# Kernel tuning notes

Hardware: AMD Instinct MI355X
Metric: run time of the kernel (lower is better)

## Reference

```python
import jax, jax.numpy as jnp
import numpy as np

B, T, DKQ, DV, EKQ, EV, H, OUT = 8, 2048, 64, 64, 128, 128, 4, 32
FF = 4 * EV
NEG = -1e30  # additive mask value (safe stand-in for -inf)


def _ln(x, g, b, eps=1e-5):
    m = x.mean(-1, keepdims=True)
    var = ((x - m) ** 2).mean(-1, keepdims=True)
    return (x - m) * jax.lax.rsqrt(var + eps) * g + b


def _attn(q, k, v, mask):
    # q,k,v: [n, T, E] -> heads [n, H, T, dh]; NOTE: no 1/sqrt(d) scaling (faithful to source)
    n, t, _ = q.shape
    q = q.reshape(n, t, H, -1).transpose(0, 2, 1, 3)
    k = k.reshape(n, t, H, -1).transpose(0, 2, 1, 3)
    v = v.reshape(n, t, H, -1).transpose(0, 2, 1, 3)
    w = jnp.einsum('bhqd,bhkd->bhqk', q, k) + mask  # [n,H,T,T]
    a = jax.nn.softmax(w, axis=-1)
    o = jnp.einsum('bhqk,bhkd->bhqd', a, v)
    return o.transpose(0, 2, 1, 3).reshape(n, t, -1)


def setup_inputs() -> dict:
    key = jax.random.key(0)
    ks = jax.random.split(key, 32)
    w = lambda k, s: jax.random.normal(k, s, jnp.float32) * 0.02
    DIN_A = DKQ + DV
    return {
        'kq': jax.random.normal(ks[0], (B, T, DKQ), jnp.float32),
        'v': jax.random.normal(ks[1], (B, T, DV), jnp.float32),
        # Layer A (input_dim = DKQ+DV, embed = EV)
        'A_Wk': w(ks[2], (DIN_A, EV)), 'A_bk': jnp.zeros((EV,), jnp.float32),
        'A_Wq': w(ks[3], (DIN_A, EV)), 'A_bq': jnp.zeros((EV,), jnp.float32),
        'A_Wv': w(ks[4], (DIN_A, EV)), 'A_bv': jnp.zeros((EV,), jnp.float32),
        'A_f1W': w(ks[5], (EV, FF)), 'A_f1b': jnp.zeros((FF,), jnp.float32),
        'A_f2W': w(ks[6], (FF, EV)), 'A_f2b': jnp.zeros((EV,), jnp.float32),
        'A_n1g': jnp.ones((EV,), jnp.float32), 'A_n1b': jnp.zeros((EV,), jnp.float32),
        'A_n2g': jnp.ones((EV,), jnp.float32), 'A_n2b': jnp.zeros((EV,), jnp.float32),
        # Layer B (kq -> EKQ, vA -> EV)
        'B_Wk': w(ks[7], (DKQ, EKQ)), 'B_bk': jnp.zeros((EKQ,), jnp.float32),
        'B_Wq': w(ks[8], (DKQ, EKQ)), 'B_bq': jnp.zeros((EKQ,), jnp.float32),
        'B_Wv': w(ks[9], (EV, EV)), 'B_bv': jnp.zeros((EV,), jnp.float32),
        'B_f1W': w(ks[10], (EV, FF)), 'B_f1b': jnp.zeros((FF,), jnp.float32),
        'B_f2W': w(ks[11], (FF, EV)), 'B_f2b': jnp.zeros((EV,), jnp.float32),
        # Output head
        'out_W': w(ks[12], (EV, OUT)), 'out_b': jnp.zeros((OUT,), jnp.float32),
    }


def reference(kq, v, A_Wk, A_bk, A_Wq, A_bq, A_Wv, A_bv, A_f1W, A_f1b, A_f2W, A_f2b,
              A_n1g, A_n1b, A_n2g, A_n2b, B_Wk, B_bk, B_Wq, B_bq, B_Wv, B_bv,
              B_f1W, B_f1b, B_f2W, B_f2b, out_W, out_b):
    n, t, _ = kq.shape
    i = jnp.arange(t)[:, None]
    j = jnp.arange(t)[None, :]
    mask_a = jnp.where(j <= i, 0.0, NEG).astype(jnp.float32)               # causal (diag=1)
    mask_b = jnp.where((j < i) | ((i == 0) & (j == 0)), 0.0, NEG).astype(jnp.float32)  # strict causal + (0,0) exception

    # ---- Layer A ----
    X = jnp.concatenate([kq, v], axis=-1)
    K = X @ A_Wk + A_bk
    Q = X @ A_Wq + A_bq
    V = X @ A_Wv + A_bv
    attn_out = _attn(Q, K, V, mask_a)
    h1 = _ln(V + attn_out, A_n1g, A_n1b)
    ff = jax.nn.gelu(h1 @ A_f1W + A_f1b, approximate=False) @ A_f2W + A_f2b
    vA = _ln(h1 + ff, A_n2g, A_n2b)

    # ---- Layer B (no residuals / norms: values is overwritten in source) ----
    K2 = kq @ B_Wk + B_bk
    Q2 = kq @ B_Wq + B_bq
    V2 = vA @ B_Wv + B_bv
    attn_out2 = _attn(Q2, K2, V2, mask_b)
    ff2 = jax.nn.gelu(attn_out2 @ B_f1W + B_f1b, approximate=False) @ B_f2W + B_f2b

    return ff2 @ out_W + out_b
```

## Files before the change

kernel.cpp:

```cpp
#include <hip/hip_runtime.h>
#include <hip/hip_bf16.h>

#define TSEQ 2048
#define NBATCH 8
#define NROWS (NBATCH*TSEQ)
#define EMB 128
#define NH 4
#define DH 32
#define OUTD 32
#define APLANE (NROWS*EMB)
#define LOG2E 1.44269504088896340736f
#define NPAR 4

typedef short s8v __attribute__((ext_vector_type(8)));
typedef short s4v __attribute__((ext_vector_type(4)));
typedef float f4v __attribute__((ext_vector_type(4)));
typedef float f16v __attribute__((ext_vector_type(16)));
typedef unsigned int u4v __attribute__((ext_vector_type(4)));

__device__ __forceinline__ unsigned short f2bf(float f){
  unsigned int u = __float_as_uint(f);
  unsigned int r = u + 0x7fffu + ((u >> 16) & 1u);
  return (unsigned short)(r >> 16);
}
__device__ __forceinline__ float bf2f(unsigned short u){
  return __uint_as_float(((unsigned int)u) << 16);
}
__device__ __forceinline__ float exp2fast(float x){
#if __has_builtin(__builtin_amdgcn_exp2f)
  return __builtin_amdgcn_exp2f(x);
#else
  return __expf(x * 0.6931471805599453f);
#endif
}

struct WPack {
  const float* src[10];
  int off[10];
  int ntk[10];
  int rowoff[10];
  int nsh[10];
  int kn[10];
};
__global__ __launch_bounds__(256) void prep(WPack p, short* __restrict__ warena,
                                            const float* __restrict__ kq, const float* __restrict__ v,
                                            unsigned short* __restrict__ X){
  int blk = blockIdx.x;
  if (blk < (NROWS*EMB/256)){
    int idx = blk*256 + threadIdx.x;
    int row = idx >> 7, c = idx & 127;
    float val = (c < 64) ? kq[row*64 + c] : v[row*64 + (c-64)];
    unsigned short hi = f2bf(val);
    X[idx]          = hi;
    X[idx + APLANE] = f2bf(val - bf2f(hi));
    return;
  }
  blk -= (NROWS*EMB/256);
  int m = 0;
  #pragma unroll
  for (int i=0;i<10;i++){
    int nb = p.kn[i] >> 8;
    if (blk < nb){ m = i; break; }
    blk -= nb;
  }
  int idx = blk*256 + threadIdx.x;
  float x = p.src[m][idx];
  int nsh = p.nsh[m];
  int n = idx & ((1<<nsh)-1);
  int k = idx >> nsh;
  int K = p.kn[m] >> nsh;
  unsigned short hi = f2bf(x);
  unsigned short lo = f2bf(x - bf2f(hi));
  short* dh = warena + p.off[m] + (size_t)(p.rowoff[m] + n)*K + k;
  dh[0]        = (short)hi;
  dh[p.ntk[m]] = (short)lo;
}

struct GOuts {
  const float* bias[3];
  float* of[3];
  unsigned short* ob[3];
  float scl[3];
};
template<int CT>
__global__ __launch_bounds__(256) void gemm2(
    const unsigned short* __restrict__ A, int aplane, int lda, int K, int niter,
    const short* __restrict__ wt, int NTK,
    GOuts og, int NT, int nseg, int act,
    unsigned short* __restrict__ vtb, int vcol0){
  __shared__ short As[2][2][64*40];
  const int tid  = threadIdx.x;
  const int w    = tid >> 6;
  const int lane = tid & 63;
  const int col  = lane & 15;
  const int quad = lane >> 4;
  const int row0 = blockIdx.x * 64;
  const int cb   = blockIdx.y*(64*CT) + w*(16*CT) + col;
  const bool two = (aplane != 0);

  f4v acc[4][CT];
  #pragma unroll
  for (int i=0;i<4;i++)
    #pragma unroll
    for (int j=0;j<CT;j++) acc[i][j] = (f4v){0.f,0.f,0.f,0.f};

  const int ar = tid >> 2, ac = (tid & 3)*8;
  const unsigned short* abase = A + (size_t)(row0 + ar)*lda;

  s8v pah, pal;
  pah = *(const s8v*)(abase + ac);
  if (two) pal = *(const s8v*)(abase + aplane + ac);

  const short* wbase[CT];
  #pragma unroll
  for (int ct=0;ct<CT;ct++) wbase[ct] = wt + (size_t)(cb + ct*16)*K + quad*8;

  for (int i=0;i<niter;i++){
    const int buf = i & 1;
    *(s8v*)&As[buf][0][ar*40 + ac] = pah;
    if (two) *(s8v*)&As[buf][1][ar*40 + ac] = pal;
    __syncthreads();
    if (i+1 < niter){
      const int kcol = (i+1)*32 + ac;
      pah = *(const s8v*)(abase + kcol);
      if (two) pal = *(const s8v*)(abase + aplane + kcol);
    }
    s8v bh[CT], bl[CT];
    #pragma unroll
    for (int ct=0;ct<CT;ct++){
      bh[ct] = *(const s8v*)(wbase[ct] + i*32);
      bl[ct] = *(const s8v*)(wbase[ct] + i*32 + NTK);
    }
    #pragma unroll
    for (int rt=0;rt<4;rt++){
      s8v ah = *(const s8v*)&As[buf][0][(rt*16 + col)*40 + quad*8];
      #pragma unroll
      for (int ct=0;ct<CT;ct++)
        acc[rt][ct] = __builtin_amdgcn_mfma_f32_16x16x32_bf16(ah, bh[ct], acc[rt][ct], 0, 0, 0);
      if (two){
        s8v al = *(const s8v*)&As[buf][1][(rt*16 + col)*40 + quad*8];
        #pragma unroll
        for (int ct=0;ct<CT;ct++)
          acc[rt][ct] = __builtin_amdgcn_mfma_f32_16x16x32_bf16(al, bh[ct], acc[rt][ct], 0, 0, 0);
      }
      #pragma unroll
      for (int ct=0;ct<CT;ct++)
        acc[rt][ct] = __builtin_amdgcn_mfma_f32_16x16x32_bf16(ah, bl[ct], acc[rt][ct], 0, 0, 0);
    }
  }

  const int NB = 64*CT;
  const int cb0 = (int)blockIdx.y * NB;
  const bool dotr = (vtb != nullptr) && (cb0 >= vcol0) && (cb0 < vcol0 + 128);
  short* Lt = &As[0][0][0];
  if (dotr) __syncthreads();

  #pragma unroll
  for (int ct=0;ct<CT;ct++){
    const int cg = cb + ct*16;
    int seg, lcol, ldc;
    if (nseg > 1){ seg = cg >> 7; lcol = cg & 127; ldc = 128; }
    else         { seg = 0; lcol = cg; ldc = NT; }
    const float bv = og.bias[seg][lcol];
    const float sc = og.scl[seg];
    float* of = og.of[seg];
    unsigned short* ob = og.ob[seg];
    #pragma unroll
    for (int rt=0;rt<4;rt++){
      s4v pk;
      #pragma unroll
      for (int r=0;r<4;r++){
        const int row = row0 + rt*16 + quad*4 + r;
        float val = acc[rt][ct][r] + bv;
        if (act == 1) val = 0.5f*val*(1.f + erff(val*0.70710678118654752440f));
        val *= sc;
        if (ob)      ob[(size_t)row*ldc + lcol] = f2bf(val);
        else if (of) of[(size_t)row*ldc + lcol] = val;
        if (dotr) pk[r] = (short)f2bf(val);
      }
      if (dotr)
        *(s4v*)&Lt[(w*(16*CT) + ct*16 + col)*72 + rt*16 + quad*4] = pk;
    }
  }
  if (dotr){
    __syncthreads();
    const int b = row0 >> 11, t0 = row0 & 2047;
    #pragma unroll
    for (int it=0; it<2*CT; it++){
      const int cl = it*32 + (tid>>3);
      const int t8 = (tid&7)*8;
      s8v o = *(const s8v*)&Lt[cl*72 + t8];
      const int cr = cb0 + cl - vcol0;
      *(s8v*)(vtb + ((size_t)((b*4 + (cr>>5))*32 + (cr&31)))*2048 + t0 + t8) = o;
    }
  }
}

#define KSTR 40
#define VSTR 72
__device__ __forceinline__ int kswz(int row, int c){ return (row*KSTR + c) ^ (((row>>3)&3)<<3); }
__device__ __forceinline__ int vswz(int row, int c){ return (row*VSTR + c) ^ (((row>>3)&3)<<3); }

__global__ __launch_bounds__(256, 4) void flash5(const unsigned short* __restrict__ Qb,
                                                 const unsigned short* __restrict__ Kb,
                                                 const unsigned short* __restrict__ Vtb,
                                                 float* __restrict__ O, float* __restrict__ L,
                                                 int mode){
  __shared__ short Kt[64*KSTR];
  __shared__ short Vt[32*VSTR];
  const int tid  = threadIdx.x;
  const int w    = tid >> 6;
  const int lane = tid & 63;
  const int q31  = lane & 31;
  const int hi   = lane >> 5;
  const int bh = blockIdx.y;
  const int b = bh >> 2, h = bh & 3;
  const int par = blockIdx.z;
  float* Op = O + (size_t)par*NROWS*EMB;
  float* Lp = L + (size_t)par*NROWS*NH;
  const int kr = tid >> 2, kc8 = (tid & 3)*8;
  const int vd = tid >> 3, vk8 = (tid & 7)*8;

  for (int pass = 0; pass < 2; pass++){
    const int qt = pass ? (int)blockIdx.x : (15 - (int)blockIdx.x);
    const int qbase = qt*128;
    const int qrow  = qbase + w*32 + q31;
    const int jtmax = 2*qt + 1;

    s8v qB0 = *(const s8v*)(Qb + (size_t)(b*TSEQ + qrow)*EMB + h*DH + hi*8);
    s8v qB1 = *(const s8v*)(Qb + (size_t)(b*TSEQ + qrow)*EMB + h*DH + 16 + hi*8);
    f16v o;
    #pragma unroll
    for (int r=0;r<16;r++) o[r] = 0.f;
    float lr = 0.f;

    if (par <= jtmax){
      s8v ka = *(const s8v*)(Kb + (size_t)(b*TSEQ + par*64 + kr)*EMB + h*DH + kc8);
      s8v va = *(const s8v*)(Vtb + ((size_t)bh*32 + vd)*TSEQ + par*64 + vk8);
      for (int jt = par; jt <= jtmax; jt += NPAR){
        __syncthreads();
        *(s8v*)&Kt[kswz(kr, kc8)] = ka;
        *(s8v*)&Vt[vswz(vd, vk8)] = va;
        __syncthreads();
        if (jt + NPAR <= jtmax){
          ka = *(const s8v*)(Kb + (size_t)(b*TSEQ + (jt+NPAR)*64 + kr)*EMB + h*DH + kc8);
          va = *(const s8v*)(Vtb + ((size_t)bh*32 + vd)*TSEQ + (jt+NPAR)*64 + vk8);
        }
        const bool domask = (jt >= 2*qt);
        #pragma unroll
        for (int kt=0;kt<2;kt++){
          f16v s;
          #pragma unroll
          for (int r=0;r<16;r++) s[r] = 0.f;
          {
            s8v kf0 = *(const s8v*)&Kt[kswz(kt*32 + q31, hi*8)];
            s = __builtin_amdgcn_mfma_f32_32x32x16_bf16(kf0, qB0, s, 0, 0, 0);
            s8v kf1 = *(const s8v*)&Kt[kswz(kt*32 + q31, 16 + hi*8)];
            s = __builtin_amdgcn_mfma_f32_32x32x16_bf16(kf1, qB1, s, 0, 0, 0);
          }
          if (domask){
            #pragma unroll
            for (int r=0;r<16;r++){
              const int jg = jt*64 + kt*32 + (r&3) + 8*(r>>2) + 4*hi;
              const bool ok = (mode==0) ? (jg <= qrow) : ((jg < qrow) || (qrow==0 && jg==0));
              s[r] = ok ? s[r] : -1e30f;
            }
          }
          #pragma unroll
          for (int r=0;r<16;r++){ float pv = exp2fast(s[r]); s[r] = pv; lr += pv; }
          unsigned P2[4][2];
          #pragma unroll
          for (int m=0;m<4;m++){
            asm("v_cvt_pk_bf16_f32 %0, %1, %2" : "=v"(P2[m][0]) : "v"(s[4*m+0]), "v"(s[4*m+1]));
            asm("v_cvt_pk_bf16_f32 %0, %1, %2" : "=v"(P2[m][1]) : "v"(s[4*m+2]), "v"(s[4*m+3]));
          }
          #pragma unroll
          for (int kcl=0;kcl<2;kcl++){
            const unsigned own0 = hi ? P2[2*kcl+1][0] : P2[2*kcl][0];
            const unsigned own1 = hi ? P2[2*kcl+1][1] : P2[2*kcl][1];
            const unsigned inv0 = hi ? P2[2*kcl][0]   : P2[2*kcl+1][0];
            const unsigned inv1 = hi ? P2[2*kcl][1]   : P2[2*kcl+1][1];
            const unsigned sx0 = (unsigned)__shfl_xor((int)inv0, 32);
            const unsigned sx1 = (unsigned)__shfl_xor((int)inv1, 32);
            u4v au;
            au[0] = hi ? sx0 : own0;  au[1] = hi ? sx1 : own1;
            au[2] = hi ? own0 : sx0;  au[3] = hi ? own1 : sx1;
            s8v af = __builtin_bit_cast(s8v, au);
            s8v vf = *(const s8v*)&Vt[vswz(q31, kt*32 + kcl*16 + hi*8)];
            o = __builtin_amdgcn_mfma_f32_32x32x16_bf16(af, vf, o, 0, 0, 0);
          }
        }
      }
    }
    const float lt = lr + __shfl_xor(lr, 32);
    #pragma unroll
    for (int r=0;r<16;r++){
      const int ql = (r&3) + 8*(r>>2) + 4*hi;
      Op[(size_t)(b*TSEQ + qbase + w*32 + ql)*EMB + h*DH + q31] = o[r];
    }
    if (hi == 0) Lp[(size_t)(b*TSEQ + qrow)*NH + h] = lt;
  }
}

__global__ __launch_bounds__(256) void combine_ln(const float* __restrict__ O, const float* __restrict__ L,
                                                  const float* __restrict__ Vf,
                                                  const float* __restrict__ g, const float* __restrict__ bt,
                                                  unsigned short* __restrict__ outp){
  const int row = blockIdx.x*4 + (threadIdx.x >> 6);
  const int tid = threadIdx.x & 63;
  const size_t base = (size_t)row*EMB;
  const int h0 = tid >> 5, h1i = 2 + (tid >> 5);
  float la = 0.f, lb = 0.f, s0 = 0.f, s1 = 0.f;
  #pragma unroll
  for (int p=0;p<NPAR;p++){
    la += L[(size_t)p*NROWS*NH + (size_t)row*NH + h0];
    lb += L[(size_t)p*NROWS*NH + (size_t)row*NH + h1i];
    s0 += O[(size_t)p*NROWS*EMB + base + tid];
    s1 += O[(size_t)p*NROWS*EMB + base + tid + 64];
  }
  float x0 = Vf[base+tid]    + s0/la;
  float x1 = Vf[base+tid+64] + s1/lb;
  float s  = x0 + x1;
  float s2 = x0*x0 + x1*x1;
  #pragma unroll
  for (int off=1; off<64; off<<=1){
    s  += __shfl_xor(s,  off);
    s2 += __shfl_xor(s2, off);
  }
  float mean = s * (1.f/128.f);
  float var  = s2 * (1.f/128.f) - mean*mean;
  float rstd = rsqrtf(var + 1e-5f);
  float y0 = (x0-mean)*rstd*g[tid]    + bt[tid];
  float y1 = (x1-mean)*rstd*g[tid+64] + bt[tid+64];
  unsigned short h0b = f2bf(y0), h1b = f2bf(y1);
  outp[base+tid]             = h0b;
  outp[base+tid+64]          = h1b;
  outp[base+tid+APLANE]      = f2bf(y0 - bf2f(h0b));
  outp[base+tid+64+APLANE]   = f2bf(y1 - bf2f(h1b));
}

__global__ __launch_bounds__(256) void ln2(const unsigned short* __restrict__ Xp, const float* __restrict__ R,
                                           const float* __restrict__ g, const float* __restrict__ bt,
                                           unsigned short* __restrict__ outp){
  const int row = blockIdx.x*4 + (threadIdx.x >> 6);
  const int tid = threadIdx.x & 63;
  const size_t base = (size_t)row*EMB;
  float x0 = bf2f(Xp[base+tid])    + bf2f(Xp[base+tid+APLANE])    + R[base+tid];
  float x1 = bf2f(Xp[base+tid+64]) + bf2f(Xp[base+tid+64+APLANE]) + R[base+tid+64];
  float s  = x0 + x1;
  float s2 = x0*x0 + x1*x1;
  #pragma unroll
  for (int off=1; off<64; off<<=1){
    s  += __shfl_xor(s,  off);
    s2 += __shfl_xor(s2, off);
  }
  float mean = s * (1.f/128.f);
  float var  = s2 * (1.f/128.f) - mean*mean;
  float rstd = rsqrtf(var + 1e-5f);
  float y0 = (x0-mean)*rstd*g[tid]    + bt[tid];
  float y1 = (x1-mean)*rstd*g[tid+64] + bt[tid+64];
  unsigned short h0b = f2bf(y0), h1b = f2bf(y1);
  outp[base+tid]             = h0b;
  outp[base+tid+64]          = h1b;
  outp[base+tid+APLANE]      = f2bf(y0 - bf2f(h0b));
  outp[base+tid+64+APLANE]   = f2bf(y1 - bf2f(h1b));
}

__global__ __launch_bounds__(256) void combine_b(const float* __restrict__ O, const float* __restrict__ L,
                                                 unsigned short* __restrict__ outp){
  const int idx = blockIdx.x*256 + threadIdx.x;
  const int row = idx >> 7, c = idx & 127, h = c >> 5;
  float l = 0.f, ov = 0.f;
  #pragma unroll
  for (int p=0;p<NPAR;p++){
    l  += L[(size_t)p*NROWS*NH + (size_t)row*NH + h];
    ov += O[(size_t)p*NROWS*EMB + idx];
  }
  const float v = ov / l;
  unsigned short hb = f2bf(v);
  outp[idx]          = hb;
  outp[idx + APLANE] = f2bf(v - bf2f(hb));
}

__global__ __launch_bounds__(256) void out_proj(const float* __restrict__ A,
                                                const float* __restrict__ W, const float* __restrict__ bb,
                                                float* __restrict__ out){
  __shared__ float As[8*128];
  __shared__ float Ws2[128*32];
  const int tid = threadIdx.x;
  const int row0 = blockIdx.x * 8;
  for (int idx = tid; idx < 8*128; idx += 256) As[idx] = A[(size_t)row0*128 + idx];
  for (int idx = tid; idx < 128*32; idx += 256) Ws2[idx] = W[idx];
  __syncthreads();
  const int r = tid >> 5, c = tid & 31;
  float acc = bb[c];
  #pragma unroll 8
  for (int k=0;k<128;k++) acc = fmaf(As[r*128 + k], Ws2[k*32 + c], acc);
  out[(size_t)(row0 + r)*OUTD + c] = acc;
}

extern "C" void kernel_launch(void* const* d_in, const int* in_sizes, int n_in,
                              void* d_out, int out_size, void* d_ws, size_t ws_size,
                              hipStream_t stream) {
  const float* kq    = (const float*)d_in[0];
  const float* v     = (const float*)d_in[1];
  const float* A_Wk  = (const float*)d_in[2];  const float* A_bk  = (const float*)d_in[3];
  const float* A_Wq  = (const float*)d_in[4];  const float* A_bq  = (const float*)d_in[5];
  const float* A_Wv  = (const float*)d_in[6];  const float* A_bv  = (const float*)d_in[7];
  const float* A_f1W = (const float*)d_in[8];  const float* A_f1b = (const float*)d_in[9];
  const float* A_f2W = (const float*)d_in[10]; const float* A_f2b = (const float*)d_in[11];
  const float* A_n1g = (const float*)d_in[12]; const float* A_n1b = (const float*)d_in[13];
  const float* A_n2g = (const float*)d_in[14]; const float* A_n2b = (const float*)d_in[15];
  const float* B_Wk  = (const float*)d_in[16]; const float* B_bk  = (const float*)d_in[17];
  const float* B_Wq  = (const float*)d_in[18]; const float* B_bq  = (const float*)d_in[19];
  const float* B_Wv  = (const float*)d_in[20]; const float* B_bv  = (const float*)d_in[21];
  const float* B_f1W = (const float*)d_in[22]; const float* B_f1b = (const float*)d_in[23];
  const float* B_f2W = (const float*)d_in[24]; const float* B_f2b = (const float*)d_in[25];
  const float* out_W = (const float*)d_in[26]; const float* out_b = (const float*)d_in[27];
  float* out = (float*)d_out;
  (void)in_sizes; (void)n_in; (void)out_size; (void)ws_size;

  char* ws = (char*)d_ws;
  const size_t MB = 1024*1024;
  short* warena = (short*)ws;
  unsigned short* Xs  = (unsigned short*)(ws + 2*MB);
  unsigned short* Qbf = (unsigned short*)(ws + 10*MB);
  unsigned short* Kbf = (unsigned short*)(ws + 14*MB);
  unsigned short* Vtb = (unsigned short*)(ws + 18*MB);
  float* Vf  = (float*)(ws + 22*MB);
  float* Opar = (float*)(ws + 30*MB);
  float* Lpar = (float*)(ws + 62*MB);
  unsigned short* h1p = (unsigned short*)(ws + 66*MB);
  unsigned short* mid = (unsigned short*)(ws + 74*MB);
  float* ffo = (float*)(ws + 90*MB);
  unsigned short* vAp = (unsigned short*)(ws + 98*MB);

  WPack p;
  const float* srcs[10] = {A_Wq,A_Wk,A_Wv,A_f1W,A_f2W,B_Wq,B_Wk,B_Wv,B_f1W,B_f2W};
  int kn[10]     = {16384,16384,16384,65536,65536,8192,8192,16384,65536,65536};
  int nsh[10]    = {7,7,7,9,7,7,7,7,9,7};
  int off[10]    = {0,0,0,98304,229376,360448,360448,393216,425984,557056};
  int ntk[10]    = {49152,49152,49152,65536,65536,16384,16384,16384,65536,65536};
  int rowoff[10] = {0,128,256,0,0,0,128,0,0,0};
  int nblk = 0;
  for (int i=0;i<10;i++){
    p.src[i]=srcs[i]; p.kn[i]=kn[i]; p.nsh[i]=nsh[i];
    p.off[i]=off[i]; p.ntk[i]=ntk[i]; p.rowoff[i]=rowoff[i];
    nblk += kn[i] >> 8;
  }
  prep<<<(NROWS*EMB/256) + nblk, 256, 0, stream>>>(p, warena, kq, v, Xs);

  GOuts oQKVA = {{A_bq,A_bk,A_bv},{nullptr,nullptr,Vf},{Qbf,Kbf,nullptr},{LOG2E,1.f,1.f}};
  GOuts oF1A  = {{A_f1b,nullptr,nullptr},{nullptr,nullptr,nullptr},{mid,nullptr,nullptr},{1.f,1.f,1.f}};
  GOuts oF2A  = {{A_f2b,nullptr,nullptr},{ffo,nullptr,nullptr},{nullptr,nullptr,nullptr},{1.f,1.f,1.f}};
  GOuts oQKB  = {{B_bq,B_bk,nullptr},{nullptr,nullptr,nullptr},{Qbf,Kbf,nullptr},{LOG2E,1.f,1.f}};
  GOuts oVB   = {{B_bv,nullptr,nullptr},{nullptr,nullptr,nullptr},{nullptr,nullptr,nullptr},{1.f,1.f,1.f}};
  GOuts oF1B  = {{B_f1b,nullptr,nullptr},{nullptr,nullptr,nullptr},{mid,nullptr,nullptr},{1.f,1.f,1.f}};
  GOuts oF2B  = {{B_f2b,nullptr,nullptr},{ffo,nullptr,nullptr},{nullptr,nullptr,nullptr},{1.f,1.f,1.f}};

  gemm2<2><<<dim3(256,3), 256, 0, stream>>>(Xs, APLANE, 128, 128, 4, warena + 0,      49152, oQKVA, 384, 3, 0, Vtb, 256);
  flash5<<<dim3(8,32,NPAR), 256, 0, stream>>>(Qbf, Kbf, Vtb, Opar, Lpar, 0);
  combine_ln<<<NROWS/4, 256, 0, stream>>>(Opar, Lpar, Vf, A_n1g, A_n1b, h1p);
  gemm2<2><<<dim3(256,4), 256, 0, stream>>>(h1p, APLANE, 128, 128, 4, warena + 98304, 65536, oF1A, 512, 1, 1, nullptr, 0);
  gemm2<1><<<dim3(256,2), 256, 0, stream>>>(mid, 0,      512, 512, 16, warena + 229376, 65536, oF2A, 128, 1, 0, nullptr, 0);
  ln2<<<NROWS/4, 256, 0, stream>>>(h1p, ffo, A_n2g, A_n2b, vAp);

  gemm2<2><<<dim3(256,2), 256, 0, stream>>>(Xs, APLANE, 128, 64, 2,  warena + 360448, 16384, oQKB, 256, 2, 0, nullptr, 0);
  gemm2<1><<<dim3(256,2), 256, 0, stream>>>(vAp, APLANE, 128, 128, 4, warena + 393216, 16384, oVB, 128, 1, 0, Vtb, 0);
  flash5<<<dim3(8,32,NPAR), 256, 0, stream>>>(Qbf, Kbf, Vtb, Opar, Lpar, 1);
  combine_b<<<NROWS*128/256, 256, 0, stream>>>(Opar, Lpar, h1p);
  gemm2<2><<<dim3(256,4), 256, 0, stream>>>(h1p, APLANE, 128, 128, 4, warena + 425984, 65536, oF1B, 512, 1, 1, nullptr, 0);
  gemm2<1><<<dim3(256,2), 256, 0, stream>>>(mid, 0,      512, 512, 16, warena + 557056, 65536, oF2B, 128, 1, 0, nullptr, 0);

  out_proj<<<NROWS/8, 256, 0, stream>>>(ffo, out_W, out_b, out);
}
```

Baseline: 305.3 us.

## Fuse FF2 GEMM with LayerNorm and output head; widen FF1 blocks to 8 waves

Adds a gemm_f2 kernel that computes the FF2 GEMM for a 64-row tile with 8 waves covering all 128 output columns, keeps the result in shared memory, and then either applies the residual add plus LayerNorm (layer A) or the 128x32 output projection (layer B). This removes the separate ln2 and out_proj kernels and the fp32 ffo round trip through global memory. FF1 GEMMs now use a templated 8-wave variant that covers 256 columns per block, halving the y-grid. The fused kernel uses more shared memory per block (about 36 KB), and its scalar output-head loop may limit occupancy.

```diff
diff --git a/kernel.cpp b/kernel.cpp
--- a/kernel.cpp
+++ b/kernel.cpp
@@ -1,5 +1,6 @@
 #include <hip/hip_runtime.h>
 #include <hip/hip_bf16.h>
+#include <type_traits>
 
 #define TSEQ 2048
 #define NBATCH 8
@@ -82,8 +83,8 @@
   unsigned short* ob[3];
   float scl[3];
 };
-template<int CT>
-__global__ __launch_bounds__(256) void gemm2(
+template<int CT, int NWV>
+__global__ __launch_bounds__(NWV*64) void gemm2(
     const unsigned short* __restrict__ A, int aplane, int lda, int K, int niter,
     const short* __restrict__ wt, int NTK,
     GOuts og, int NT, int nseg, int act,
@@ -95,7 +96,7 @@
   const int col  = lane & 15;
   const int quad = lane >> 4;
   const int row0 = blockIdx.x * 64;
-  const int cb   = blockIdx.y*(64*CT) + w*(16*CT) + col;
+  const int cb   = blockIdx.y*(NWV*16*CT) + w*(16*CT) + col;
   const bool two = (aplane != 0);
 
   f4v acc[4][CT];
@@ -104,12 +105,14 @@
     #pragma unroll
     for (int j=0;j<CT;j++) acc[i][j] = (f4v){0.f,0.f,0.f,0.f};
 
-  const int ar = tid >> 2, ac = (tid & 3)*8;
+  using sv = typename std::conditional<NWV==4, s8v, s4v>::type;
+  const int ar = (NWV==4) ? (tid >> 2) : (tid >> 3);
+  const int ac = (NWV==4) ? ((tid & 3)*8) : ((tid & 7)*4);
   const unsigned short* abase = A + (size_t)(row0 + ar)*lda;
 
-  s8v pah, pal;
-  pah = *(const s8v*)(abase + ac);
-  if (two) pal = *(const s8v*)(abase + aplane + ac);
+  sv pah, pal;
+  pah = *(const sv*)(abase + ac);
+  if (two) pal = *(const sv*)(abase + aplane + ac);
 
   const short* wbase[CT];
   #pragma unroll
@@ -117,13 +120,13 @@
 
   for (int i=0;i<niter;i++){
     const int buf = i & 1;
-    *(s8v*)&As[buf][0][ar*40 + ac] = pah;
-    if (two) *(s8v*)&As[buf][1][ar*40 + ac] = pal;
+    *(sv*)&As[buf][0][ar*40 + ac] = pah;
+    if (two) *(sv*)&As[buf][1][ar*40 + ac] = pal;
     __syncthreads();
     if (i+1 < niter){
       const int kcol = (i+1)*32 + ac;
-      pah = *(const s8v*)(abase + kcol);
-      if (two) pal = *(const s8v*)(abase + aplane + kcol);
+      pah = *(const sv*)(abase + kcol);
+      if (two) pal = *(const sv*)(abase + aplane + kcol);
     }
     s8v bh[CT], bl[CT];
     #pragma unroll
@@ -149,9 +152,10 @@
     }
   }
 
-  const int NB = 64*CT;
+  const int NB = NWV*16*CT;
   const int cb0 = (int)blockIdx.y * NB;
-  const bool dotr = (vtb != nullptr) && (cb0 >= vcol0) && (cb0 < vcol0 + 128);
+  bool dotr = false;
+  if (NWV == 4) dotr = (vtb != nullptr) && (cb0 >= vcol0) && (cb0 < vcol0 + 128);
   short* Lt = &As[0][0][0];
   if (dotr) __syncthreads();
 
@@ -182,17 +186,122 @@
         *(s4v*)&Lt[(w*(16*CT) + ct*16 + col)*72 + rt*16 + quad*4] = pk;
     }
   }
-  if (dotr){
+  if (NWV == 4){
+    if (dotr){
+      __syncthreads();
+      const int b = row0 >> 11, t0 = row0 & 2047;
+      #pragma unroll
+      for (int it=0; it<2*CT; it++){
+        const int cl = it*32 + (tid>>3);
+        const int t8 = (tid&7)*8;
+        s8v o = *(const s8v*)&Lt[cl*72 + t8];
+        const int cr = cb0 + cl - vcol0;
+        *(s8v*)(vtb + ((size_t)((b*4 + (cr>>5))*32 + (cr&31)))*2048 + t0 + t8) = o;
+      }
+    }
+  }
+}
+
+template<int MODE>
+__global__ __launch_bounds__(512) void gemm_f2(
+    const unsigned short* __restrict__ A,
+    const short* __restrict__ wt, int NTK,
+    const float* __restrict__ bias,
+    const unsigned short* __restrict__ resid,
+    const float* __restrict__ g, const float* __restrict__ bt,
+    unsigned short* __restrict__ outp,
+    const float* __restrict__ Wo, const float* __restrict__ bo,
+    float* __restrict__ outhead){
+  __shared__ short As[2][64*40];
+  __shared__ float Lf[64*132];
+  __shared__ float Ws2[128*32];
+  const int tid  = threadIdx.x;
+  const int w    = tid >> 6;
+  const int lane = tid & 63;
+  const int col  = lane & 15;
+  const int quad = lane >> 4;
+  const int row0 = blockIdx.x * 64;
+  const int cg   = w*16 + col;
+
+  if (MODE == 1){
+    for (int idx = tid; idx < 128*32; idx += 512) Ws2[idx] = Wo[idx];
+  }
+
+  f4v acc[4];
+  #pragma unroll
+  for (int i=0;i<4;i++) acc[i] = (f4v){0.f,0.f,0.f,0.f};
+
+  const int ar = tid >> 3, ac = (tid & 7)*4;
+  const unsigned short* abase = A + (size_t)(row0 + ar)*512;
+  s4v pa = *(const s4v*)(abase + ac);
+  const short* wb = wt + (size_t)cg*512 + quad*8;
+
+  for (int i=0;i<16;i++){
+    const int buf = i & 1;
+    *(s4v*)&As[buf][ar*40 + ac] = pa;
     __syncthreads();
-    const int b = row0 >> 11, t0 = row0 & 2047;
-    #pragma unroll
-    for (int it=0; it<2*CT; it++){
-      const int cl = it*32 + (tid>>3);
-      const int t8 = (tid&7)*8;
-      s8v o = *(const s8v*)&Lt[cl*72 + t8];
-      const int cr = cb0 + cl - vcol0;
-      *(s8v*)(vtb + ((size_t)((b*4 + (cr>>5))*32 + (cr&31)))*2048 + t0 + t8) = o;
-    }
+    if (i+1 < 16) pa = *(const s4v*)(abase + (i+1)*32 + ac);
+    s8v bh = *(const s8v*)(wb + i*32);
+    s8v bl = *(const s8v*)(wb + i*32 + NTK);
+    #pragma unroll
+    for (int rt=0;rt<4;rt++){
+      s8v ah = *(const s8v*)&As[buf][(rt*16 + col)*40 + quad*8];
+      acc[rt] = __builtin_amdgcn_mfma_f32_16x16x32_bf16(ah, bh, acc[rt], 0, 0, 0);
+      acc[rt] = __builtin_amdgcn_mfma_f32_16x16x32_bf16(ah, bl, acc[rt], 0, 0, 0);
+    }
+  }
+
+  const float bv = bias[cg];
+  #pragma unroll
+  for (int rt=0;rt<4;rt++){
+    #pragma unroll
+    for (int r=0;r<4;r++){
+      const int row = rt*16 + quad*4 + r;
+      Lf[row*132 + cg] = acc[rt][r] + bv;
+    }
+  }
+  __syncthreads();
+
+  if (MODE == 0){
+    for (int rr=0; rr<8; rr++){
+      const int row = w*8 + rr;
+      const size_t gbase = (size_t)(row0 + row)*EMB;
+      float x0 = Lf[row*132 + lane]
+               + bf2f(resid[gbase+lane])    + bf2f(resid[gbase+lane+APLANE]);
+      float x1 = Lf[row*132 + lane + 64]
+               + bf2f(resid[gbase+lane+64]) + bf2f(resid[gbase+lane+64+APLANE]);
+      float s  = x0 + x1;
+      float s2 = x0*x0 + x1*x1;
+      #pragma unroll
+      for (int off=1; off<64; off<<=1){
+        s  += __shfl_xor(s,  off);
+        s2 += __shfl_xor(s2, off);
+      }
+      float mean = s * (1.f/128.f);
+      float var  = s2 * (1.f/128.f) - mean*mean;
+      float rstd = rsqrtf(var + 1e-5f);
+      float y0 = (x0-mean)*rstd*g[lane]    + bt[lane];
+      float y1 = (x1-mean)*rstd*g[lane+64] + bt[lane+64];
+      unsigned short h0b = f2bf(y0), h1b = f2bf(y1);
+      outp[gbase+lane]             = h0b;
+      outp[gbase+lane+64]          = h1b;
+      outp[gbase+lane+APLANE]      = f2bf(y0 - bf2f(h0b));
+      outp[gbase+lane+64+APLANE]   = f2bf(y1 - bf2f(h1b));
+    }
+  } else {
+    const int row = tid >> 3, c0 = (tid & 7)*4;
+    f4v a4;
+    #pragma unroll
+    for (int j=0;j<4;j++) a4[j] = bo[c0+j];
+    #pragma unroll 16
+    for (int k=0;k<128;k++){
+      const float av = Lf[row*132 + k];
+      #pragma unroll
+      for (int j=0;j<4;j++) a4[j] = fmaf(av, Ws2[k*32 + c0 + j], a4[j]);
+    }
+    float* op = outhead + (size_t)(row0 + row)*OUTD + c0;
+    #pragma unroll
+    for (int j=0;j<4;j++) op[j] = a4[j];
   }
 }
 
@@ -339,33 +448,6 @@
   outp[base+tid+64+APLANE]   = f2bf(y1 - bf2f(h1b));
 }
 
-__global__ __launch_bounds__(256) void ln2(const unsigned short* __restrict__ Xp, const float* __restrict__ R,
-                                           const float* __restrict__ g, const float* __restrict__ bt,
-                                           unsigned short* __restrict__ outp){
-  const int row = blockIdx.x*4 + (threadIdx.x >> 6);
-  const int tid = threadIdx.x & 63;
-  const size_t base = (size_t)row*EMB;
-  float x0 = bf2f(Xp[base+tid])    + bf2f(Xp[base+tid+APLANE])    + R[base+tid];
-  float x1 = bf2f(Xp[base+tid+64]) + bf2f(Xp[base+tid+64+APLANE]) + R[base+tid+64];
-  float s  = x0 + x1;
-  float s2 = x0*x0 + x1*x1;
-  #pragma unroll
-  for (int off=1; off<64; off<<=1){
-    s  += __shfl_xor(s,  off);
-    s2 += __shfl_xor(s2, off);
-  }
-  float mean = s * (1.f/128.f);
-  float var  = s2 * (1.f/128.f) - mean*mean;
-  float rstd = rsqrtf(var + 1e-5f);
-  float y0 = (x0-mean)*rstd*g[tid]    + bt[tid];
-  float y1 = (x1-mean)*rstd*g[tid+64] + bt[tid+64];
-  unsigned short h0b = f2bf(y0), h1b = f2bf(y1);
-  outp[base+tid]             = h0b;
-  outp[base+tid+64]          = h1b;
-  outp[base+tid+APLANE]      = f2bf(y0 - bf2f(h0b));
-  outp[base+tid+64+APLANE]   = f2bf(y1 - bf2f(h1b));
-}
-
 __global__ __launch_bounds__(256) void combine_b(const float* __restrict__ O, const float* __restrict__ L,
                                                  unsigned short* __restrict__ outp){
   const int idx = blockIdx.x*256 + threadIdx.x;
@@ -380,23 +462,6 @@
   unsigned short hb = f2bf(v);
   outp[idx]          = hb;
   outp[idx + APLANE] = f2bf(v - bf2f(hb));
-}
-
-__global__ __launch_bounds__(256) void out_proj(const float* __restrict__ A,
-                                                const float* __restrict__ W, const float* __restrict__ bb,
-                                                float* __restrict__ out){
-  __shared__ float As[8*128];
-  __shared__ float Ws2[128*32];
-  const int tid = threadIdx.x;
-  const int row0 = blockIdx.x * 8;
-  for (int idx = tid; idx < 8*128; idx += 256) As[idx] = A[(size_t)row0*128 + idx];
-  for (int idx = tid; idx < 128*32; idx += 256) Ws2[idx] = W[idx];
-  __syncthreads();
-  const int r = tid >> 5, c = tid & 31;
-  float acc = bb[c];
-  #pragma unroll 8
-  for (int k=0;k<128;k++) acc = fmaf(As[r*128 + k], Ws2[k*32 + c], acc);
-  out[(size_t)(row0 + r)*OUTD + c] = acc;
 }
 
 extern "C" void kernel_launch(void* const* d_in, const int* in_sizes, int n_in,
@@ -432,8 +497,7 @@
   float* Lpar = (float*)(ws + 62*MB);
   unsigned short* h1p = (unsigned short*)(ws + 66*MB);
   unsigned short* mid = (unsigned short*)(ws + 74*MB);
-  float* ffo = (float*)(ws + 90*MB);
-  unsigned short* vAp = (unsigned short*)(ws + 98*MB);
+  unsigned short* vAp = (unsigned short*)(ws + 90*MB);
 
   WPack p;
   const float* srcs[10] = {A_Wq,A_Wk,A_Wv,A_f1W,A_f2W,B_Wq,B_Wk,B_Wv,B_f1W,B_f2W};
@@ -452,25 +516,22 @@
 
   GOuts oQKVA = {{A_bq,A_bk,A_bv},{nullptr,nullptr,Vf},{Qbf,Kbf,nullptr},{LOG2E,1.f,1.f}};
   GOuts oF1A  = {{A_f1b,nullptr,nullptr},{nullptr,nullptr,nullptr},{mid,nullptr,nullptr},{1.f,1.f,1.f}};
-  GOuts oF2A  = {{A_f2b,nullptr,nullptr},{ffo,nullptr,nullptr},{nullptr,nullptr,nullptr},{1.f,1.f,1.f}};
   GOuts oQKB  = {{B_bq,B_bk,nullptr},{nullptr,nullptr,nullptr},{Qbf,Kbf,nullptr},{LOG2E,1.f,1.f}};
-  GOuts oVB   = {{B_bv,nullptr,nullptr},{nullptr,nullptr,nullptr},{nullptr,nullptr,nullptr},{1.f,1.f,1.f}};
+  GOuts oVB   = {{B_bv,nullptr,nullptr},{nullptr,nullptr,nullptr},{nullptr,nullptr,nullptr}, {1.f,1.f,1.f}};
   GOuts oF1B  = {{B_f1b,nullptr,nullptr},{nullptr,nullptr,nullptr},{mid,nullptr,nullptr},{1.f,1.f,1.f}};
-  GOuts oF2B  = {{B_f2b,nullptr,nullptr},{ffo,nullptr,nullptr},{nullptr,nullptr,nullptr},{1.f,1.f,1.f}};
-
-  gemm2<2><<<dim3(256,3), 256, 0, stream>>>(Xs, APLANE, 128, 128, 4, warena + 0,      49152, oQKVA, 384, 3, 0, Vtb, 256);
+
+  gemm2<2,4><<<dim3(256,3), 256, 0, stream>>>(Xs, APLANE, 128, 128, 4, warena + 0,      49152, oQKVA, 384, 3, 0, Vtb, 256);
   flash5<<<dim3(8,32,NPAR), 256, 0, stream>>>(Qbf, Kbf, Vtb, Opar, Lpar, 0);
   combine_ln<<<NROWS/4, 256, 0, stream>>>(Opar, Lpar, Vf, A_n1g, A_n1b, h1p);
-  gemm2<2><<<dim3(256,4), 256, 0, stream>>>(h1p, APLANE, 128, 128, 4, warena + 98304, 65536, oF1A, 512, 1, 1, nullptr, 0);
-  gemm2<1><<<dim3(256,2), 256, 0, stream>>>(mid, 0,      512, 512, 16, warena + 229376, 65536, oF2A, 128, 1, 0, nullptr, 0);
-  ln2<<<NROWS/4, 256, 0, stream>>>(h1p, ffo, A_n2g, A_n2b, vAp);
-
-  gemm2<2><<<dim3(256,2), 256, 0, stream>>>(Xs, APLANE, 128, 64, 2,  warena + 360448, 16384, oQKB, 256, 2, 0, nullptr, 0);
-  gemm2<1><<<dim3(256,2), 256, 0, stream>>>(vAp, APLANE, 128, 128, 4, warena + 393216, 16384, oVB, 128, 1, 0, Vtb, 0);
+  gemm2<2,8><<<dim3(256,2), 512, 0, stream>>>(h1p, APLANE, 128, 128, 4, warena + 98304, 65536, oF1A, 512, 1, 1, nullptr, 0);
+  gemm_f2<0><<<256, 512, 0, stream>>>(mid, warena + 229376, 65536, A_f2b,
+                                      h1p, A_n2g, A_n2b, vAp, nullptr, nullptr, nullptr);
+
+  gemm2<2,4><<<dim3(256,2), 256, 0, stream>>>(Xs, APLANE, 128, 64, 2,  warena + 360448, 16384, oQKB, 256, 2, 0, nullptr, 0);
+  gemm2<1,4><<<dim3(256,2), 256, 0, stream>>>(vAp, APLANE, 128, 128, 4, warena + 393216, 16384, oVB, 128, 1, 0, Vtb, 0);
   flash5<<<dim3(8,32,NPAR), 256, 0, stream>>>(Qbf, Kbf, Vtb, Opar, Lpar, 1);
   combine_b<<<NROWS*128/256, 256, 0, stream>>>(Opar, Lpar, h1p);
-  gemm2<2><<<dim3(256,4), 256, 0, stream>>>(h1p, APLANE, 128, 128, 4, warena + 425984, 65536, oF1B, 512, 1, 1, nullptr, 0);
-  gemm2<1><<<dim3(256,2), 256, 0, stream>>>(mid, 0,      512, 512, 16, warena + 557056, 65536, oF2B, 128, 1, 0, nullptr, 0);
-
-  out_proj<<<NROWS/8, 256, 0, stream>>>(ffo, out_W, out_b, out);
-}
+  gemm2<2,8><<<dim3(256,2), 512, 0, stream>>>(h1p, APLANE, 128, 128, 4, warena + 425984, 65536, oF1B, 512, 1, 1, nullptr, 0);
+  gemm_f2<1><<<256, 512, 0, stream>>>(mid, warena + 557056, 65536, B_f2b,
+                                      nullptr, nullptr, nullptr, nullptr, out_W, out_b, out);
+}
```

After: 286.1 us. 6.3% less time.
